# Kernel tuning notes

Hardware: AMD Instinct MI355X
Metric: run time of the kernel (lower is better)

Reference implementation:

```python
import jax, jax.numpy as jnp
import numpy as np

DIM = 768; HEADS = 12; DIM_HEAD = 64; INNER = HEADS * DIM_HEAD
GT_HEADS = 8; GT_DH = 64; GT_INNER = GT_HEADS * GT_DH
W = 128; DEPTH = 4; NUM_TOKENS = 32000; SEQ = 4096; MAX_SEQ = 4096; B = 1
FF_MULT = 4


def layer_norm(x, g, b, eps=1e-5):
    mu = x.mean(-1, keepdims=True)
    var = ((x - mu) ** 2).mean(-1, keepdims=True)
    return (x - mu) / jnp.sqrt(var + eps) * g + b


def ffn(x, w1_, b1_, w2_, b2_):
    return jax.nn.gelu(x @ w1_ + b1_, approximate=False) @ w2_ + b2_


def global_attn(g, wqkv, wo_, bo_):
    # full causal MHA over the (few) global tokens
    b, n, _ = g.shape
    q, k, v = jnp.split(g @ wqkv, 3, axis=-1)
    sh = lambda t: t.reshape(b, n, GT_HEADS, GT_DH).transpose(0, 2, 1, 3)  # b h n d
    q, k, v = sh(q), sh(k), sh(v)
    sim = jnp.einsum('bhid,bhjd->bhij', q, k) * (GT_DH ** -0.5)
    cm = jnp.triu(jnp.ones((n, n), dtype=bool), k=1)
    sim = jnp.where(cm, -jnp.finfo(sim.dtype).max, sim)
    attn = jax.nn.softmax(sim, axis=-1)
    out = jnp.einsum('bhij,bhjd->bhid', attn, v)
    out = out.transpose(0, 2, 1, 3).reshape(b, n, GT_INNER)
    return out @ wo_ + bo_


def local_attn(x, g, wq_, wkv_, wo_, bo_):
    # windowed look-back attention + global-token keys. n assumed multiple of W.
    b, n, _ = x.shape
    bh = b * HEADS
    buckets = n // W
    sh = lambda t, m: t.reshape(b, m, HEADS, DIM_HEAD).transpose(0, 2, 1, 3).reshape(bh, m, DIM_HEAD)
    q = sh(x @ wq_, n)
    k, v = jnp.split(x @ wkv_, 2, axis=-1)
    k, v = sh(k, n), sh(v, n)
    win = lambda t: t.reshape(bh, buckets, W, DIM_HEAD)
    q, k, v = win(q), win(k), win(v)
    kp = jnp.pad(k, ((0, 0), (1, 0), (0, 0), (0, 0)))
    # NOTE: faithfully replicates upstream bug -- the lambda in the torch code
    # builds BOTH k and v from k, so v becomes the k look-back concat too.
    k2 = jnp.concatenate([kp[:, :-1], kp[:, 1:]], axis=2)  # [bh, buckets, 2W, d]
    v2 = k2
    local_j = 2 * W
    # global tokens (last one dropped)
    gt = g[:, :-1]
    ng = gt.shape[1]
    gk, gv = jnp.split(gt @ wkv_, 2, axis=-1)
    gsh = lambda t: t.reshape(b, ng, HEADS, DIM_HEAD).transpose(0, 2, 1, 3).reshape(bh, ng, DIM_HEAD)
    gk = jnp.broadcast_to(gsh(gk)[:, None], (bh, buckets, ng, DIM_HEAD))
    gv = jnp.broadcast_to(gsh(gv)[:, None], (bh, buckets, ng, DIM_HEAD))
    kf = jnp.concatenate([gk, k2], axis=2)
    vf = jnp.concatenate([gv, v2], axis=2)
    sim = jnp.einsum('bwid,bwjd->bwij', q, kf) * (DIM_HEAD ** -0.5)
    mv = -jnp.finfo(sim.dtype).max
    m_local = jnp.triu(jnp.ones((W, local_j), dtype=bool), k=local_j - W + 1)
    m_local = jnp.broadcast_to(m_local[None], (buckets, W, local_j))
    m_glob = jnp.triu(jnp.ones((buckets, ng), dtype=bool), k=ng - W)
    m_glob = jnp.broadcast_to(m_glob[:, None, :], (buckets, W, ng))
    cmask = jnp.concatenate([m_glob, m_local], axis=-1)[None]
    sim = jnp.where(cmask, mv, sim)
    attn = jax.nn.softmax(sim, axis=-1)
    out = jnp.einsum('bwij,bwjd->bwid', attn, vf)
    out = out.reshape(b, HEADS, n, DIM_HEAD).transpose(0, 2, 1, 3).reshape(b, n, INNER)
    return out @ wo_ + bo_


def setup_inputs() -> dict:
    ks = iter(jax.random.split(jax.random.key(0), 64))
    nrm = lambda shape: jax.random.normal(next(ks), shape, jnp.float32) * 0.02
    return {
        'x': jax.random.randint(next(ks), (B, SEQ), 0, NUM_TOKENS),
        'token_emb': nrm((NUM_TOKENS, DIM)),
        'pos_emb': nrm((MAX_SEQ, DIM)),
        'global_pos_emb': nrm((MAX_SEQ // W, DIM)),
        'gt_ln1_g': jnp.ones((DIM,)), 'gt_ln1_b': jnp.zeros((DIM,)),
        'gt_wqkv': nrm((DIM, 3 * GT_INNER)), 'gt_wo': nrm((GT_INNER, DIM)), 'gt_bo': jnp.zeros((DIM,)),
        'gt_ln2_g': jnp.ones((DIM,)), 'gt_ln2_b': jnp.zeros((DIM,)),
        'gt_w1': nrm((DIM, FF_MULT * DIM)), 'gt_b1': jnp.zeros((FF_MULT * DIM,)),
        'gt_w2': nrm((FF_MULT * DIM, DIM)), 'gt_b2': jnp.zeros((DIM,)),
        'ln1_g': jnp.ones((DEPTH, DIM)), 'ln1_b': jnp.zeros((DEPTH, DIM)),
        'wq': nrm((DEPTH, DIM, INNER)), 'wkv': nrm((DEPTH, DIM, 2 * INNER)),
        'wo': nrm((DEPTH, INNER, DIM)), 'bo': jnp.zeros((DEPTH, DIM)),
        'ln2_g': jnp.ones((DEPTH, DIM)), 'ln2_b': jnp.zeros((DEPTH, DIM)),
        'w1': nrm((DEPTH, DIM, FF_MULT * DIM)), 'b1': jnp.zeros((DEPTH, FF_MULT * DIM)),
        'w2': nrm((DEPTH, FF_MULT * DIM, DIM)), 'b2': jnp.zeros((DEPTH, DIM)),
        'f_ln_g': jnp.ones((DIM,)), 'f_ln_b': jnp.zeros((DIM,)),
        'w_logits': nrm((DIM, NUM_TOKENS)), 'b_logits': jnp.zeros((NUM_TOKENS,)),
    }


def reference(x, token_emb, pos_emb, global_pos_emb,
              gt_ln1_g, gt_ln1_b, gt_wqkv, gt_wo, gt_bo,
              gt_ln2_g, gt_ln2_b, gt_w1, gt_b1, gt_w2, gt_b2,
              ln1_g, ln1_b, wq, wkv, wo, bo,
              ln2_g, ln2_b, w1, b1, w2, b2,
              f_ln_g, f_ln_b, w_logits, b_logits):
    b, n = x.shape
    buckets = n // W  # n % W == 0 for chosen shapes -> r = 0 branch
    h = token_emb[x]                                    # [b, n, dim]
    g = h.reshape(b, buckets, W, DIM).mean(axis=2)      # pooled global tokens
    h = h + pos_emb[:n][None]
    g = g + global_pos_emb[:buckets][None]
    for l in range(DEPTH):
        g = g + global_attn(layer_norm(g, gt_ln1_g, gt_ln1_b), gt_wqkv, gt_wo, gt_bo)
        g = g + ffn(layer_norm(g, gt_ln2_g, gt_ln2_b), gt_w1, gt_b1, gt_w2, gt_b2)
        h = h + local_attn(layer_norm(h, ln1_g[l], ln1_b[l]), g, wq[l], wkv[l], wo[l], bo[l])
        h = h + ffn(layer_norm(h, ln2_g[l], ln2_b[l]), w1[l], b1[l], w2[l], b2[l])
    return layer_norm(h, f_ln_g, f_ln_b) @ w_logits + b_logits
```

## Files before the change

### kernel.cpp

```cpp
#include <hip/hip_runtime.h>
#include <hip/hip_bf16.h>


#define DIMM   768
#define SEQLEN 4096
#define NHEADS 12
#define DH     64
#define WWIN   128
#define NBUCK  32
#define NDEPTH 4
#define FFDIM  3072
#define NTOK   32000
#define QKLD   1536
#define NEG_MAX (-3.402823466e38f)

typedef unsigned short u16;
typedef __attribute__((ext_vector_type(8))) short bf16x8;
typedef __attribute__((ext_vector_type(4))) float f32x4;

#define GLOAD16(gp, lp) \
  __builtin_amdgcn_global_load_lds((const __attribute__((address_space(1))) void*)(gp), \
                                   (__attribute__((address_space(3))) void*)(lp), 16, 0, 0)

#define BAR()      __builtin_amdgcn_s_barrier()
#define SBAR()     __builtin_amdgcn_sched_barrier(0)
#define PRIO(x)    __builtin_amdgcn_s_setprio(x)
#define VMDRAIN()  asm volatile("s_waitcnt vmcnt(0)" ::: "memory")

__global__ __launch_bounds__(256) void embed_kernel(
    const int* __restrict__ x, const float* __restrict__ tok,
    const float* __restrict__ pos, float* __restrict__ h) {
  int row = blockIdx.x;
  int t = threadIdx.x;
  int tk = x[row];
  const float* te = tok + (size_t)tk * DIMM;
  const float* pe = pos + (size_t)row * DIMM;
  float* hr = h + (size_t)row * DIMM;
  hr[t]       = te[t]       + pe[t];
  hr[t + 256] = te[t + 256] + pe[t + 256];
  hr[t + 512] = te[t + 512] + pe[t + 512];
}

__global__ __launch_bounds__(256) void ln_kernel(
    const float* __restrict__ in, const float* __restrict__ gam,
    const float* __restrict__ bet, __hip_bfloat16* __restrict__ out) {
  int row = blockIdx.x;
  int t = threadIdx.x;
  const float* xr = in + (size_t)row * DIMM;
  float v0 = xr[t], v1 = xr[t + 256], v2 = xr[t + 512];
  float s  = v0 + v1 + v2;
  float s2 = v0 * v0 + v1 * v1 + v2 * v2;
  #pragma unroll
  for (int o = 32; o > 0; o >>= 1) {
    s  += __shfl_down(s, o);
    s2 += __shfl_down(s2, o);
  }
  __shared__ float red[2][4];
  int wid = t >> 6, lane = t & 63;
  if (lane == 0) { red[0][wid] = s; red[1][wid] = s2; }
  __syncthreads();
  if (t == 0) {
    float ts  = red[0][0] + red[0][1] + red[0][2] + red[0][3];
    float ts2 = red[1][0] + red[1][1] + red[1][2] + red[1][3];
    float mean = ts * (1.0f / DIMM);
    float var  = ts2 * (1.0f / DIMM) - mean * mean;
    red[0][0] = mean;
    red[1][0] = rsqrtf(var + 1e-5f);
  }
  __syncthreads();
  float mean = red[0][0], rstd = red[1][0];
  __hip_bfloat16* orow = out + (size_t)row * DIMM;
  orow[t]       = __float2bfloat16((v0 - mean) * rstd * gam[t]       + bet[t]);
  orow[t + 256] = __float2bfloat16((v1 - mean) * rstd * gam[t + 256] + bet[t + 256]);
  orow[t + 512] = __float2bfloat16((v2 - mean) * rstd * gam[t + 512] + bet[t + 512]);
}

__global__ __launch_bounds__(256) void wprep_kernel(
    const float* __restrict__ src, u16* __restrict__ dst,
    int ldsrc, int Krows, size_t sls, size_t dls) {
  __shared__ float tile[32][33];
  int l = blockIdx.z;
  int n0 = blockIdx.x * 32, k0 = blockIdx.y * 32;
  int tx = threadIdx.x & 31, ty = threadIdx.x >> 5;
  const float* s = src + (size_t)l * sls;
  u16* d = dst + (size_t)l * dls;
  #pragma unroll
  for (int i = 0; i < 4; ++i)
    tile[ty + i * 8][tx] = s[(size_t)(k0 + ty + i * 8) * ldsrc + n0 + tx];
  __syncthreads();
  #pragma unroll
  for (int i = 0; i < 4; ++i) {
    __hip_bfloat16 b = __float2bfloat16(tile[tx][ty + i * 8]);
    d[(size_t)(n0 + ty + i * 8) * Krows + k0 + tx] = *(u16*)&b;
  }
}

template<int TBM, int TBN>
__global__ __launch_bounds__(256) void gemm_bf16(
    const u16* __restrict__ A, const u16* __restrict__ Bt,
    const float* __restrict__ bias, const float* __restrict__ resid,
    void* __restrict__ Cv, int K, int ldc, int act, int cbf16) {
  constexpr int MFR = TBM / 32;
  constexpr int NFR = TBN / 32;
  constexpr int G = (TBM == 128 ? 2 : 1) + (TBN == 128 ? 2 : 1);
  __shared__ u16 As[2][TBM * 32];
  __shared__ u16 Bs[2][TBN * 32];
  int tid = threadIdx.x;
  int wave = tid >> 6, lane = tid & 63;

  int lin = blockIdx.y * gridDim.x + blockIdx.x;
  int cpx = (gridDim.x * gridDim.y) >> 3;
  int swz = (lin & 7) * cpx + (lin >> 3);
  int by = swz % gridDim.y;
  int bx = swz / gridDim.y;

  int bm = by * TBM, bn = bx * TBN;
  int wm = (wave >> 1) * (TBM / 2), wn = (wave & 1) * (TBN / 2);
  int fr = lane & 15, fq = lane >> 4;

  f32x4 acc[MFR][NFR];
  #pragma unroll
  for (int i = 0; i < MFR; ++i)
    #pragma unroll
    for (int j = 0; j < NFR; ++j) acc[i][j] = (f32x4){0.f, 0.f, 0.f, 0.f};

  int r0 = tid >> 2;
  int kb = ((tid & 3) ^ ((r0 >> 1) & 3)) * 8;
  const u16* aptr = A + (size_t)(bm + r0) * K + kb;
  const u16* bptr = Bt + (size_t)(bn + r0) * K + kb;
  int sA = (fq ^ ((fr >> 1) & 3)) * 8;

#define STAGE_TILE(buf) do {                                          \
    char* lA = (char*)(&As[buf][0]) + wave * 1024;                    \
    char* lB = (char*)(&Bs[buf][0]) + wave * 1024;                    \
    GLOAD16(aptr, lA);                                                \
    if constexpr (TBM == 128) GLOAD16(aptr + (size_t)64 * K, lA + 4096); \
    GLOAD16(bptr, lB);                                                \
    if constexpr (TBN == 128) GLOAD16(bptr + (size_t)64 * K, lB + 4096); \
    aptr += 32; bptr += 32;                                           \
  } while (0)

  const int nk = K >> 5;
  STAGE_TILE(0);
  STAGE_TILE(1);

  for (int t = 0; t < nk; ++t) {
    const int cur = t & 1;
    if (t + 1 < nk) {
      if constexpr (G == 2) asm volatile("s_waitcnt vmcnt(2)" ::: "memory");
      else if constexpr (G == 3) asm volatile("s_waitcnt vmcnt(3)" ::: "memory");
      else asm volatile("s_waitcnt vmcnt(4)" ::: "memory");
    } else {
      VMDRAIN();
    }
    BAR();
    bf16x8 af[MFR], bfr[NFR];
    #pragma unroll
    for (int m = 0; m < MFR; ++m)
      af[m] = *(const bf16x8*)&As[cur][(wm + m * 16 + fr) * 32 + sA];
    #pragma unroll
    for (int n = 0; n < NFR; ++n)
      bfr[n] = *(const bf16x8*)&Bs[cur][(wn + n * 16 + fr) * 32 + sA];
    asm volatile("s_waitcnt lgkmcnt(0)" ::: "memory");
    SBAR();
    BAR();
    if (t + 2 < nk) STAGE_TILE(cur);
    PRIO(1);
    #pragma unroll
    for (int m = 0; m < MFR; ++m)
      #pragma unroll
      for (int n = 0; n < NFR; ++n)
        acc[m][n] = __builtin_amdgcn_mfma_f32_16x16x32_bf16(af[m], bfr[n], acc[m][n], 0, 0, 0);
    PRIO(0);
  }
#undef STAGE_TILE

  #pragma unroll
  for (int m = 0; m < MFR; ++m) {
    #pragma unroll
    for (int rr = 0; rr < 4; ++rr) {
      int row = bm + wm + m * 16 + fq * 4 + rr;
      #pragma unroll
      for (int n = 0; n < NFR; ++n) {
        int col = bn + wn + n * 16 + fr;
        float v = acc[m][n][rr];
        if (bias) v += bias[col];
        if (act) v = 0.5f * v * (1.0f + erff(v * 0.70710678118654752f));
        if (resid) v += resid[(size_t)row * ldc + col];
        if (cbf16) {
          __hip_bfloat16 b = __float2bfloat16(v);
          ((u16*)Cv)[(size_t)row * ldc + col] = *(u16*)&b;
        } else {
          ((float*)Cv)[(size_t)row * ldc + col] = v;
        }
      }
    }
  }
}

__global__ __launch_bounds__(512, 1) void gemm256(
    const u16* __restrict__ A, const u16* __restrict__ Bt,
    const float* __restrict__ bias, float* __restrict__ C, int K, int ldc) {
  __shared__ __align__(16) char GL[131072];
  const int tid = threadIdx.x;
  const int wave = tid >> 6, lane = tid & 63;
  const int fr = lane & 15, fq = lane >> 4;

  int lin = blockIdx.y * gridDim.x + blockIdx.x;
  int cpx = (gridDim.x * gridDim.y) >> 3;
  int swz = (lin & 7) * cpx + (lin >> 3);
  int by = swz % gridDim.y;
  int bx = swz / gridDim.y;

  const int bm = by * 256, bn = bx * 256;
  const int wm = (wave >> 2) * 128, wn = (wave & 3) * 64;

  const int r_in = tid >> 2;
  const int g_swz = (tid & 3) ^ ((r_in >> 1) & 3);
  const size_t a_base = (size_t)(bm + r_in) * K + g_swz * 8;
  const size_t b_base = (size_t)(bn + r_in) * K + g_swz * 8;
  const int lds_st = wave * 1024;

  const int sA = (fq ^ ((fr >> 1) & 3)) * 16;

  f32x4 acc[8][4];
  #pragma unroll
  for (int i = 0; i < 8; ++i)
    #pragma unroll
    for (int j = 0; j < 4; ++j) acc[i][j] = (f32x4){0.f, 0.f, 0.f, 0.f};

#define STG(s, b) do {                                                  \
    const u16* ga = A + a_base + (size_t)(s) * 32;                      \
    const u16* gb = Bt + b_base + (size_t)(s) * 32;                     \
    GLOAD16(ga,                   GL + (b) * 16384 + lds_st);           \
    GLOAD16(ga + (size_t)128 * K, GL + (b) * 16384 + 8192 + lds_st);    \
    GLOAD16(gb,                   GL + 65536 + (b) * 16384 + lds_st);   \
    GLOAD16(gb + (size_t)128 * K, GL + 65536 + (b) * 16384 + 8192 + lds_st); \
  } while (0)

  const int nk = K >> 5;
  STG(0, 0);
  STG(1, 1);
  STG(2, 2);

  for (int t = 0; t < nk; ++t) {
    const int buf = t & 3;
    if (t <= nk - 3)      asm volatile("s_waitcnt vmcnt(8)" ::: "memory");
    else if (t == nk - 2) asm volatile("s_waitcnt vmcnt(4)" ::: "memory");
    else                  VMDRAIN();
    BAR();
    if (t + 3 < nk) STG(t + 3, (t + 3) & 3);
    bf16x8 aq[8], bq[4];
    const char* pa = GL + buf * 16384;
    const char* pb = GL + 65536 + buf * 16384;
    #pragma unroll
    for (int m = 0; m < 8; ++m)
      aq[m] = *(const bf16x8*)(pa + (wm + m * 16 + fr) * 64 + sA);
    #pragma unroll
    for (int n = 0; n < 4; ++n)
      bq[n] = *(const bf16x8*)(pb + (wn + n * 16 + fr) * 64 + sA);
    asm volatile("s_waitcnt lgkmcnt(0)" ::: "memory");
    SBAR();
    PRIO(1);
    #pragma unroll
    for (int m = 0; m < 8; ++m)
      #pragma unroll
      for (int n = 0; n < 4; ++n)
        acc[m][n] = __builtin_amdgcn_mfma_f32_16x16x32_bf16(aq[m], bq[n], acc[m][n], 0, 0, 0);
    PRIO(0);
  }
#undef STG

  #pragma unroll
  for (int m = 0; m < 8; ++m) {
    #pragma unroll
    for (int rr = 0; rr < 4; ++rr) {
      int row = bm + wm + m * 16 + fq * 4 + rr;
      #pragma unroll
      for (int n = 0; n < 4; ++n) {
        int col = bn + wn + n * 16 + fr;
        C[(size_t)row * ldc + col] = acc[m][n][rr] + bias[col];
      }
    }
  }
}

__global__ __launch_bounds__(256, 1) void attn_mfma(
    const u16* __restrict__ QK, u16* __restrict__ CTX) {
  __shared__ __align__(16) char LDS[131072];
  char* Kl = LDS;
  char* Kt = LDS + 32768;
  const int w = blockIdx.x, hd = blockIdx.y;
  const int tid = threadIdx.x;
  const int wave = tid >> 6, lane = tid & 63;
  const int fr = lane & 15, fq = lane >> 4;
  char* Pw = LDS + 65536 + wave * 16384;

  {
    const int j = tid;
    const int p = (w - 1) * WWIN + j;
    bf16x8 kv[8];
    if (p >= 0) {
      const bf16x8* src = (const bf16x8*)(QK + (size_t)p * QKLD + DIMM + hd * DH);
      #pragma unroll
      for (int g = 0; g < 8; ++g) kv[g] = src[g];
    } else {
      #pragma unroll
      for (int g = 0; g < 8; ++g) kv[g] = (bf16x8){0, 0, 0, 0, 0, 0, 0, 0};
    }
    #pragma unroll
    for (int g = 0; g < 8; ++g)
      *(bf16x8*)(Kl + j * 128 + ((g ^ (j & 7)) * 16)) = kv[g];
    #pragma unroll
    for (int g = 0; g < 8; ++g)
      #pragma unroll
      for (int e = 0; e < 8; ++e) {
        const int d = g * 8 + e;
        *(u16*)(Kt + d * 512 + (((j >> 3) ^ (d & 7)) * 16) + ((j & 7) * 2)) =
            (u16)kv[g][e];
      }
  }

  bf16x8 aq[2][2];
  #pragma unroll
  for (int m = 0; m < 2; ++m)
    #pragma unroll
    for (int kk = 0; kk < 2; ++kk)
      aq[m][kk] = *(const bf16x8*)(QK +
          (size_t)(w * WWIN + wave * 32 + m * 16 + fr) * QKLD + hd * DH + kk * 32 + fq * 8);

  __syncthreads();

  f32x4 sacc[2][16];
  #pragma unroll
  for (int m = 0; m < 2; ++m)
    #pragma unroll
    for (int n = 0; n < 16; ++n) sacc[m][n] = (f32x4){0.f, 0.f, 0.f, 0.f};
  #pragma unroll
  for (int n = 0; n < 16; ++n) {
    #pragma unroll
    for (int kk = 0; kk < 2; ++kk) {
      bf16x8 bk = *(const bf16x8*)(Kl + (n * 16 + fr) * 128 +
                                   (((kk * 4 + fq) ^ (fr & 7)) * 16));
      #pragma unroll
      for (int m = 0; m < 2; ++m)
        sacc[m][n] = __builtin_amdgcn_mfma_f32_16x16x32_bf16(aq[m][kk], bk, sacc[m][n], 0, 0, 0);
    }
  }

  float inv_[2][4];
  #pragma unroll
  for (int m = 0; m < 2; ++m) {
    #pragma unroll
    for (int rr = 0; rr < 4; ++rr) {
      const int r = wave * 32 + m * 16 + fq * 4 + rr;
      float pv[16];
      float mx = NEG_MAX;
      #pragma unroll
      for (int n = 0; n < 16; ++n) {
        const int j = n * 16 + fr;
        float s = sacc[m][n][rr] * 0.125f;
        bool vis = (j <= r + 128);
        pv[n] = vis ? s : NEG_MAX;
        if (vis) mx = fmaxf(mx, s);
      }
      #pragma unroll
      for (int o = 1; o < 16; o <<= 1) mx = fmaxf(mx, __shfl_xor(mx, o));
      float sum = 0.f;
      #pragma unroll
      for (int n = 0; n < 16; ++n) {
        float p = (pv[n] != NEG_MAX) ? __expf(pv[n] - mx) : 0.f;
        pv[n] = p;
        sum += p;
      }
      #pragma unroll
      for (int o = 1; o < 16; o <<= 1) sum += __shfl_xor(sum, o);
      inv_[m][rr] = 1.0f / sum;
      const int rl = m * 16 + fq * 4 + rr;
      #pragma unroll
      for (int n = 0; n < 16; ++n) {
        __hip_bfloat16 b = __float2bfloat16(pv[n]);
        const int gj = n * 2 + (fr >> 3);
        *(u16*)(Pw + rl * 512 + ((gj ^ (rl & 7)) * 16) + ((fr & 7) * 2)) = *(u16*)&b;
      }
    }
  }
  __syncthreads();

  f32x4 oacc[2][4];
  #pragma unroll
  for (int m = 0; m < 2; ++m)
    #pragma unroll
    for (int nd = 0; nd < 4; ++nd) oacc[m][nd] = (f32x4){0.f, 0.f, 0.f, 0.f};
  #pragma unroll
  for (int kc = 0; kc < 8; ++kc) {
    const int slot = ((kc * 4 + fq) ^ (fr & 7)) * 16;
    bf16x8 pa[2];
    #pragma unroll
    for (int m = 0; m < 2; ++m)
      pa[m] = *(const bf16x8*)(Pw + (m * 16 + fr) * 512 + slot);
    #pragma unroll
    for (int nd = 0; nd < 4; ++nd) {
      bf16x8 kb = *(const bf16x8*)(Kt + (nd * 16 + fr) * 512 + slot);
      #pragma unroll
      for (int m = 0; m < 2; ++m)
        oacc[m][nd] = __builtin_amdgcn_mfma_f32_16x16x32_bf16(pa[m], kb, oacc[m][nd], 0, 0, 0);
    }
  }

  #pragma unroll
  for (int m = 0; m < 2; ++m)
    #pragma unroll
    for (int nd = 0; nd < 4; ++nd)
      #pragma unroll
      for (int rr = 0; rr < 4; ++rr) {
        const int row = w * WWIN + wave * 32 + m * 16 + fq * 4 + rr;
        const int col = hd * DH + nd * 16 + fr;
        __hip_bfloat16 b = __float2bfloat16(oacc[m][nd][rr] * inv_[m][rr]);
        CTX[(size_t)row * DIMM + col] = *(u16*)&b;
      }
}

extern "C" void kernel_launch(void* const* d_in, const int* in_sizes, int n_in,
                              void* d_out, int out_size, void* d_ws, size_t ws_size,
                              hipStream_t stream) {
  const int*   x         = (const int*)d_in[0];
  const float* token_emb = (const float*)d_in[1];
  const float* pos_emb   = (const float*)d_in[2];
  const float* ln1_g = (const float*)d_in[15];
  const float* ln1_b = (const float*)d_in[16];
  const float* wq    = (const float*)d_in[17];
  const float* wkv   = (const float*)d_in[18];
  const float* wo    = (const float*)d_in[19];
  const float* bo    = (const float*)d_in[20];
  const float* ln2_g = (const float*)d_in[21];
  const float* ln2_b = (const float*)d_in[22];
  const float* w1    = (const float*)d_in[23];
  const float* b1    = (const float*)d_in[24];
  const float* w2    = (const float*)d_in[25];
  const float* b2    = (const float*)d_in[26];
  const float* f_ln_g = (const float*)d_in[27];
  const float* f_ln_b = (const float*)d_in[28];
  const float* w_logits = (const float*)d_in[29];
  const float* b_logits = (const float*)d_in[30];
  float* out = (float*)d_out;

  char* ob = (char*)d_out;
  float* h    = (float*)(ob + 0);
  u16* qk     = (u16*)(ob + 12582912);
  u16* ctx    = (u16*)(ob + 25165824);
  u16* mid    = (u16*)(ob + 31457280);
  u16* warena = (u16*)(ob + 56623104);
  const size_t WQ_SZ = (size_t)DIMM * DIMM;
  const size_t W1_SZ = (size_t)DIMM * FFDIM;
  const size_t LW = 3 * WQ_SZ + 2 * W1_SZ;
  u16* qkw_t = warena;
  u16* wo_t  = warena + 2 * WQ_SZ;
  u16* w1_t  = warena + 3 * WQ_SZ;
  u16* w2_t  = warena + 3 * WQ_SZ + W1_SZ;

  u16* wlog_t = (u16*)d_ws;
  __hip_bfloat16* lnbuf = (__hip_bfloat16*)((char*)d_ws + 49152000);

  wprep_kernel<<<dim3(24, 24, 4), 256, 0, stream>>>(wq,  qkw_t,         DIMM,   DIMM,  WQ_SZ,   LW);
  wprep_kernel<<<dim3(24, 24, 4), 256, 0, stream>>>(wkv, qkw_t + WQ_SZ, 2*DIMM, DIMM,  2*WQ_SZ, LW);
  wprep_kernel<<<dim3(24, 24, 4), 256, 0, stream>>>(wo,  wo_t,          DIMM,   DIMM,  WQ_SZ,   LW);
  wprep_kernel<<<dim3(96, 24, 4), 256, 0, stream>>>(w1,  w1_t,          FFDIM,  DIMM,  W1_SZ,   LW);
  wprep_kernel<<<dim3(24, 96, 4), 256, 0, stream>>>(w2,  w2_t,          DIMM,   FFDIM, W1_SZ,   LW);
  wprep_kernel<<<dim3(1000, 24, 1), 256, 0, stream>>>(w_logits, wlog_t, NTOK, DIMM, 0, 0);

  embed_kernel<<<SEQLEN, 256, 0, stream>>>(x, token_emb, pos_emb, h);

  for (int l = 0; l < NDEPTH; ++l) {
    ln_kernel<<<SEQLEN, 256, 0, stream>>>(h, ln1_g + l * DIMM, ln1_b + l * DIMM, lnbuf);
    gemm_bf16<64, 128><<<dim3(12, 64), 256, 0, stream>>>(
        (const u16*)lnbuf, qkw_t + l * LW, nullptr, nullptr, qk, DIMM, QKLD, 0, 1);
    attn_mfma<<<dim3(NBUCK, NHEADS), 256, 0, stream>>>(qk, ctx);
    gemm_bf16<64, 64><<<dim3(12, 64), 256, 0, stream>>>(
        ctx, wo_t + l * LW, bo + l * DIMM, h, h, DIMM, DIMM, 0, 0);
    ln_kernel<<<SEQLEN, 256, 0, stream>>>(h, ln2_g + l * DIMM, ln2_b + l * DIMM, lnbuf);
    gemm_bf16<64, 128><<<dim3(24, 64), 256, 0, stream>>>(
        (const u16*)lnbuf, w1_t + l * LW, b1 + l * FFDIM, nullptr, mid, DIMM, FFDIM, 1, 1);
    gemm_bf16<64, 64><<<dim3(12, 64), 256, 0, stream>>>(
        mid, w2_t + l * LW, b2 + l * DIMM, h, h, FFDIM, DIMM, 0, 0);
  }

  ln_kernel<<<SEQLEN, 256, 0, stream>>>(h, f_ln_g, f_ln_b, lnbuf);
  gemm256<<<dim3(NTOK / 256, SEQLEN / 256), 512, 0, stream>>>(
      (const u16*)lnbuf, wlog_t, b_logits, out, DIMM, NTOK);
}
```

Measured before the change: 1.155 ms.

## Shrink logits GEMM tile to 128x256 with double-buffered LDS for higher occupancy

Replaces the 256x256-tile, 4-stage-pipelined logits GEMM with a 128x256 tile using two small LDS buffers (48KB) and launch bounds allowing several blocks per CU. It aims to raise occupancy and grid size so latency is hidden by concurrent blocks rather than deep prefetch. It trades away per-block data reuse and the deeper pipeline, and adds an extra barrier per k-step.

```diff
diff --git a/kernel.cpp b/kernel.cpp
--- a/kernel.cpp
+++ b/kernel.cpp
@@ -198,10 +198,11 @@
   }
 }
 
-__global__ __launch_bounds__(512, 1) void gemm256(
+__global__ __launch_bounds__(512, 4) void gemm512(
     const u16* __restrict__ A, const u16* __restrict__ Bt,
     const float* __restrict__ bias, float* __restrict__ C, int K, int ldc) {
-  __shared__ __align__(16) char GL[131072];
+  __shared__ u16 As[2][128 * 32];
+  __shared__ u16 Bs[2][256 * 32];
   const int tid = threadIdx.x;
   const int wave = tid >> 6, lane = tid & 63;
   const int fr = lane & 15, fq = lane >> 4;
@@ -212,67 +213,62 @@
   int by = swz % gridDim.y;
   int bx = swz / gridDim.y;
 
-  const int bm = by * 256, bn = bx * 256;
-  const int wm = (wave >> 2) * 128, wn = (wave & 3) * 64;
-
-  const int r_in = tid >> 2;
-  const int g_swz = (tid & 3) ^ ((r_in >> 1) & 3);
-  const size_t a_base = (size_t)(bm + r_in) * K + g_swz * 8;
-  const size_t b_base = (size_t)(bn + r_in) * K + g_swz * 8;
-  const int lds_st = wave * 1024;
-
-  const int sA = (fq ^ ((fr >> 1) & 3)) * 16;
-
-  f32x4 acc[8][4];
-  #pragma unroll
-  for (int i = 0; i < 8; ++i)
+  const int bm = by * 128, bn = bx * 256;
+  const int wm = (wave >> 2) * 64, wn = (wave & 3) * 64;
+
+  f32x4 acc[4][4];
+  #pragma unroll
+  for (int i = 0; i < 4; ++i)
     #pragma unroll
     for (int j = 0; j < 4; ++j) acc[i][j] = (f32x4){0.f, 0.f, 0.f, 0.f};
 
-#define STG(s, b) do {                                                  \
-    const u16* ga = A + a_base + (size_t)(s) * 32;                      \
-    const u16* gb = Bt + b_base + (size_t)(s) * 32;                     \
-    GLOAD16(ga,                   GL + (b) * 16384 + lds_st);           \
-    GLOAD16(ga + (size_t)128 * K, GL + (b) * 16384 + 8192 + lds_st);    \
-    GLOAD16(gb,                   GL + 65536 + (b) * 16384 + lds_st);   \
-    GLOAD16(gb + (size_t)128 * K, GL + 65536 + (b) * 16384 + 8192 + lds_st); \
+  const int r0 = tid >> 2;
+  const int kb = ((tid & 3) ^ ((r0 >> 1) & 3)) * 8;
+  const u16* aptr = A + (size_t)(bm + r0) * K + kb;
+  const u16* bptr = Bt + (size_t)(bn + r0) * K + kb;
+  const int sA = (fq ^ ((fr >> 1) & 3)) * 8;
+
+#define STG512(buf) do {                                              \
+    char* lA = (char*)(&As[buf][0]) + wave * 1024;                    \
+    char* lB = (char*)(&Bs[buf][0]) + wave * 1024;                    \
+    GLOAD16(aptr, lA);                                                \
+    GLOAD16(bptr, lB);                                                \
+    GLOAD16(bptr + (size_t)128 * K, lB + 8192);                       \
+    aptr += 32; bptr += 32;                                           \
   } while (0)
 
   const int nk = K >> 5;
-  STG(0, 0);
-  STG(1, 1);
-  STG(2, 2);
+  STG512(0);
+  STG512(1);
 
   for (int t = 0; t < nk; ++t) {
-    const int buf = t & 3;
-    if (t <= nk - 3)      asm volatile("s_waitcnt vmcnt(8)" ::: "memory");
-    else if (t == nk - 2) asm volatile("s_waitcnt vmcnt(4)" ::: "memory");
-    else                  VMDRAIN();
+    const int cur = t & 1;
+    if (t + 1 < nk) asm volatile("s_waitcnt vmcnt(3)" ::: "memory");
+    else            VMDRAIN();
     BAR();
-    if (t + 3 < nk) STG(t + 3, (t + 3) & 3);
-    bf16x8 aq[8], bq[4];
-    const char* pa = GL + buf * 16384;
-    const char* pb = GL + 65536 + buf * 16384;
-    #pragma unroll
-    for (int m = 0; m < 8; ++m)
-      aq[m] = *(const bf16x8*)(pa + (wm + m * 16 + fr) * 64 + sA);
+    bf16x8 af[4], bq[4];
+    #pragma unroll
+    for (int m = 0; m < 4; ++m)
+      af[m] = *(const bf16x8*)&As[cur][(wm + m * 16 + fr) * 32 + sA];
     #pragma unroll
     for (int n = 0; n < 4; ++n)
-      bq[n] = *(const bf16x8*)(pb + (wn + n * 16 + fr) * 64 + sA);
+      bq[n] = *(const bf16x8*)&Bs[cur][(wn + n * 16 + fr) * 32 + sA];
     asm volatile("s_waitcnt lgkmcnt(0)" ::: "memory");
     SBAR();
+    BAR();
+    if (t + 2 < nk) STG512(cur);
     PRIO(1);
     #pragma unroll
-    for (int m = 0; m < 8; ++m)
+    for (int m = 0; m < 4; ++m)
       #pragma unroll
       for (int n = 0; n < 4; ++n)
-        acc[m][n] = __builtin_amdgcn_mfma_f32_16x16x32_bf16(aq[m], bq[n], acc[m][n], 0, 0, 0);
+        acc[m][n] = __builtin_amdgcn_mfma_f32_16x16x32_bf16(af[m], bq[n], acc[m][n], 0, 0, 0);
     PRIO(0);
   }
-#undef STG
-
-  #pragma unroll
-  for (int m = 0; m < 8; ++m) {
+#undef STG512
+
+  #pragma unroll
+  for (int m = 0; m < 4; ++m) {
     #pragma unroll
     for (int rr = 0; rr < 4; ++rr) {
       int row = bm + wm + m * 16 + fq * 4 + rr;
@@ -486,6 +482,6 @@
   }
 
   ln_kernel<<<SEQLEN, 256, 0, stream>>>(h, f_ln_g, f_ln_b, lnbuf);
-  gemm256<<<dim3(NTOK / 256, SEQLEN / 256), 512, 0, stream>>>(
+  gemm512<<<dim3(NTOK / 256, SEQLEN / 128), 512, 0, stream>>>(
       (const u16*)lnbuf, wlog_t, b_logits, out, DIMM, NTOK);
 }
```

Result: slower. 1.179 ms (+2.1%).
